# Kernel tuning notes

Measured on AMD Instinct MI355X. Metric: run time of the kernel, lower is better.

The kernel has to match this reference:

```python
import jax, jax.numpy as jnp
import numpy as np

N_NODES = 50000


def gcn_conv(x, edge_index, edge_weight, W, b):
    """PyG GCNConv: x' = D^{-1/2}(A+I)D^{-1/2} (x W) + b, with edge weights."""
    n = x.shape[0]
    x = x @ W  # transform first (PyG order): [N, d_out]
    row, col = edge_index[0], edge_index[1]  # source -> target
    # add self loops with weight 1
    loop = jnp.arange(n)
    row = jnp.concatenate([row, loop])
    col = jnp.concatenate([col, loop])
    ew = jnp.concatenate([edge_weight, jnp.ones((n,), dtype=x.dtype)])
    # symmetric normalization based on (weighted) in-degree at targets
    deg = jax.ops.segment_sum(ew, col, num_segments=n)
    dis = jnp.where(deg > 0, jax.lax.rsqrt(deg), 0.0)
    norm = dis[row] * ew * dis[col]  # [E+N]
    # gather-scale-scatter aggregation
    msg = x[row] * norm[:, None]  # [E+N, d_out]
    out = jax.ops.segment_sum(msg, col, num_segments=n)
    return out + b


def setup_inputs() -> dict:
    key = jax.random.key(0)
    ks = jax.random.split(key, 9)
    E = 800000
    bert_output = jax.random.normal(ks[0], (N_NODES, 1024), dtype=jnp.float32)
    edge_index = jax.random.randint(ks[1], (2, E), 0, N_NODES, dtype=jnp.int64)
    edge_weight = jax.random.uniform(ks[2], (E,), dtype=jnp.float32)
    s1 = 1.0 / np.sqrt(1024)
    s2 = 1.0 / np.sqrt(512)
    s3 = 1.0 / np.sqrt(128)
    W1 = jax.random.uniform(ks[3], (1024, 512), jnp.float32, -s1, s1)
    b1 = jnp.zeros((512,), jnp.float32)
    W2 = jax.random.uniform(ks[4], (512, 128), jnp.float32, -s2, s2)
    b2 = jnp.zeros((128,), jnp.float32)
    Wfc = jax.random.uniform(ks[5], (128, 14), jnp.float32, -s3, s3)
    bfc = jax.random.uniform(ks[6], (14,), jnp.float32, -s3, s3)
    return {
        "bert_output": bert_output,
        "edge_index": edge_index,
        "edge_weight": edge_weight,
        "W1": W1, "b1": b1, "W2": W2, "b2": b2, "Wfc": Wfc, "bfc": bfc,
    }


def reference(bert_output, edge_index, edge_weight, W1, b1, W2, b2, Wfc, bfc):
    h = jax.nn.relu(gcn_conv(bert_output, edge_index, edge_weight, W1, b1))
    h = jax.nn.relu(gcn_conv(h, edge_index, edge_weight, W2, b2))
    logits = h @ Wfc + bfc
    return jax.nn.sigmoid(logits)
```

## Files before the change

kernel.cpp:

```cpp
#include <hip/hip_runtime.h>
#include <stdint.h>

__device__ __forceinline__ float bf2f(unsigned short h) {
  union { uint32_t u; float f; } v; v.u = ((uint32_t)h) << 16; return v.f;
}
__device__ __forceinline__ unsigned short f2bf(float f) {
  union { float f; uint32_t u; } v; v.f = f;
  uint32_t u = v.u;
  u += 0x7FFFu + ((u >> 16) & 1u);
  return (unsigned short)(u >> 16);
}
__device__ __forceinline__ uint32_t pack2bf(float a, float b) {
  return (uint32_t)f2bf(a) | ((uint32_t)f2bf(b) << 16);
}

typedef __attribute__((ext_vector_type(8))) short short8;
typedef __attribute__((ext_vector_type(4))) float floatx4;

__device__ __forceinline__ void gl2lds16(const unsigned short* g, unsigned short* l) {
  __builtin_amdgcn_global_load_lds(
      (const __attribute__((address_space(1))) uint32_t*)(const void*)g,
      (__attribute__((address_space(3))) uint32_t*)(void*)l,
      16, 0, 0);
}

__global__ void bgcn_probe(const uint32_t* __restrict__ xw,
                           const uint32_t* __restrict__ iw,
                           int* __restrict__ flags) {
  if (threadIdx.x == 0 && blockIdx.x == 0) {
    int hits = 0;
    for (int i = 0; i < 256; ++i) {
      uint32_t b = (xw[i] >> 8) & 0x7F;
      if (b >= 0x38 && b <= 0x41) hits++;
    }
    flags[0] = (hits < 128) ? 1 : 0;
    int nz = 0;
    for (int i = 1; i < 128; i += 2) nz += (iw[i] != 0);
    flags[1] = (nz == 0) ? 1 : 0;
  }
}

__global__ void bgcn_cvt_f(const void* __restrict__ src, unsigned short* __restrict__ dst,
                           int n, const int* __restrict__ flags) {
  int i = blockIdx.x * 256 + threadIdx.x;
  if (i >= n) return;
  if (flags[0]) dst[i] = f2bf(((const float*)src)[i]);
  else          dst[i] = ((const unsigned short*)src)[i];
}
__global__ void bgcn_cvt8(const void* __restrict__ src, unsigned short* __restrict__ dst,
                          int n8, const int* __restrict__ flags) {
  int i = blockIdx.x * 256 + threadIdx.x;
  if (i >= n8) return;
  size_t o = (size_t)i * 8;
  uint4 d;
  if (flags[0]) {
    const float4* f = (const float4*)((const float*)src + o);
    float4 f0 = f[0], f1 = f[1];
    d = make_uint4(pack2bf(f0.x, f0.y), pack2bf(f0.z, f0.w),
                   pack2bf(f1.x, f1.y), pack2bf(f1.z, f1.w));
  } else {
    d = *(const uint4*)((const unsigned short*)src + o);
  }
  *(uint4*)(dst + o) = d;
}
__global__ void bgcn_cvt_i(const void* __restrict__ src, int* __restrict__ dst,
                           int n, const int* __restrict__ flags) {
  int i = blockIdx.x * 256 + threadIdx.x;
  if (i >= n) return;
  if (flags[1]) dst[i] = (int)((const long long*)src)[i];
  else          dst[i] = ((const int*)src)[i];
}
__global__ void bgcn_cvt_t(const void* __restrict__ src, unsigned short* __restrict__ dst,
                           int kbits, int N, int total, const int* __restrict__ flags) {
  int i = blockIdx.x * 256 + threadIdx.x;
  if (i >= total) return;
  int K = 1 << kbits;
  int n = i >> kbits;
  int k = i & (K - 1);
  size_t s = (size_t)k * N + n;
  if (flags[0]) dst[i] = f2bf(((const float*)src)[s]);
  else          dst[i] = ((const unsigned short*)src)[s];
}

__global__ void bgcn_init_deg(float* __restrict__ deg, int n) {
  int i = blockIdx.x * 256 + threadIdx.x;
  if (i < n) deg[i] = 1.0f;
}
__global__ void bgcn_deg(const int* __restrict__ col, const unsigned short* __restrict__ ew,
                         float* __restrict__ deg, int E) {
  int e = blockIdx.x * 256 + threadIdx.x;
  if (e < E) atomicAdd(&deg[col[e]], bf2f(ew[e]));
}
__global__ void bgcn_dis(const float* __restrict__ deg, float* __restrict__ dis, int n) {
  int i = blockIdx.x * 256 + threadIdx.x;
  if (i < n) dis[i] = rsqrtf(deg[i]);
}

__global__ void bgcn_hist(const int* __restrict__ col, int* __restrict__ counts, int E) {
  int e = blockIdx.x * 256 + threadIdx.x;
  if (e < E) atomicAdd(&counts[col[e]], 1);
}
__global__ void bgcn_scan_block(const int* __restrict__ counts, int* __restrict__ rowptr,
                                int* __restrict__ blocksum, int n) {
  __shared__ int buf[1024];
  int gid = blockIdx.x * 1024 + threadIdx.x;
  int v = (gid < n) ? counts[gid] : 0;
  buf[threadIdx.x] = v;
  __syncthreads();
  for (int off = 1; off < 1024; off <<= 1) {
    int x = (threadIdx.x >= off) ? buf[threadIdx.x - off] : 0;
    __syncthreads();
    buf[threadIdx.x] += x;
    __syncthreads();
  }
  if (gid < n) rowptr[gid + 1] = buf[threadIdx.x];
  if (threadIdx.x == 1023) blocksum[blockIdx.x] = buf[1023];
}
__global__ void bgcn_scan_tops(int* __restrict__ blocksum, int nb) {
  if (threadIdx.x == 0 && blockIdx.x == 0) {
    int acc = 0;
    for (int i = 0; i < nb; ++i) { int v = blocksum[i]; blocksum[i] = acc; acc += v; }
  }
}
__global__ void bgcn_scan_add(int* __restrict__ rowptr, const int* __restrict__ blocksum, int n) {
  int gid = blockIdx.x * 1024 + threadIdx.x;
  if (gid < n) rowptr[gid + 1] += blocksum[blockIdx.x];
  if (gid == 0) rowptr[0] = 0;
}
__global__ void bgcn_scatter(const int* __restrict__ row, const int* __restrict__ col,
                             const unsigned short* __restrict__ ew,
                             const float* __restrict__ dis,
                             const int* __restrict__ rowptr, int* __restrict__ fill,
                             int* __restrict__ esrc, float* __restrict__ enorm, int E) {
  int e = blockIdx.x * 256 + threadIdx.x;
  if (e >= E) return;
  int r = row[e], c = col[e];
  int pos = rowptr[c] + atomicAdd(&fill[c], 1);
  esrc[pos]  = r;
  enorm[pos] = dis[r] * bf2f(ew[e]) * dis[c];
}

__global__ __launch_bounds__(256) void bgcn_gemm_lds(
    const unsigned short* __restrict__ A,
    const unsigned short* __restrict__ Bt,
    unsigned short* __restrict__ C,
    int M, int N, int K, int nblk_bits) {
  __shared__ unsigned short Abuf[128 * 32];
  __shared__ unsigned short Bbuf[128 * 32];
  int t = threadIdx.x;
  int wave = t >> 6, lane = t & 63;
  int bx = blockIdx.x;
  int nblk = bx & ((1 << nblk_bits) - 1);
  int mblk = bx >> nblk_bits;
  int m0 = mblk * 128, n0 = nblk * 128;

  floatx4 acc[4][4];
  #pragma unroll
  for (int i = 0; i < 4; ++i)
    #pragma unroll
    for (int j = 0; j < 4; ++j)
      #pragma unroll
      for (int r = 0; r < 4; ++r) acc[i][j][r] = 0.0f;

  int rii  = lane >> 2;
  int koff = (lane & 3) * 8;
  int ar0 = m0 + wave * 32 + rii;      if (ar0 >= M) ar0 = M - 1;
  int ar1 = m0 + wave * 32 + 16 + rii; if (ar1 >= M) ar1 = M - 1;
  const unsigned short* Ag0 = A + (size_t)ar0 * K + koff;
  const unsigned short* Ag1 = A + (size_t)ar1 * K + koff;
  const unsigned short* Bg0 = Bt + (size_t)(n0 + wave * 32 + rii) * K + koff;
  const unsigned short* Bg1 = Bg0 + (size_t)16 * K;
  unsigned short* Al0 = Abuf + (wave * 32) * 32 + lane * 8;
  unsigned short* Al1 = Abuf + (wave * 32 + 16) * 32 + lane * 8;
  unsigned short* Bl0 = Bbuf + (wave * 32) * 32 + lane * 8;
  unsigned short* Bl1 = Bbuf + (wave * 32 + 16) * 32 + lane * 8;

  int fr = lane & 15;
  int fk = (lane >> 4) * 8;
  int mw = (wave & 1) * 64;
  int nw = (wave >> 1) * 64;

  for (int k0 = 0; k0 < K; k0 += 32) {
    gl2lds16(Ag0 + k0, Al0);
    gl2lds16(Ag1 + k0, Al1);
    gl2lds16(Bg0 + k0, Bl0);
    gl2lds16(Bg1 + k0, Bl1);
    __syncthreads();

    short8 afr[4], bfr[4];
    #pragma unroll
    for (int i = 0; i < 4; ++i)
      afr[i] = *(const short8*)(Abuf + (mw + i * 16 + fr) * 32 + fk);
    #pragma unroll
    for (int i = 0; i < 4; ++i)
      bfr[i] = *(const short8*)(Bbuf + (nw + i * 16 + fr) * 32 + fk);
    #pragma unroll
    for (int mt = 0; mt < 4; ++mt)
      #pragma unroll
      for (int nt = 0; nt < 4; ++nt)
        acc[mt][nt] = __builtin_amdgcn_mfma_f32_16x16x32_bf16(afr[mt], bfr[nt], acc[mt][nt], 0, 0, 0);
    __syncthreads();
  }

  int col_l = lane & 15;
  int row_b = (lane >> 4) * 4;
  #pragma unroll
  for (int mt = 0; mt < 4; ++mt)
    #pragma unroll
    for (int nt = 0; nt < 4; ++nt)
      #pragma unroll
      for (int r = 0; r < 4; ++r) {
        int m = m0 + mw + mt * 16 + row_b + r;
        if (m < M)
          C[(size_t)m * N + n0 + nw + nt * 16 + col_l] = f2bf(acc[mt][nt][r]);
      }
}

#define GST 40
__global__ __launch_bounds__(256, 2) void bgcn_gemm128(
    const void* __restrict__ Araw, int a_probe, const int* __restrict__ flags,
    const unsigned short* __restrict__ Bt,
    unsigned short* __restrict__ C,
    int M, int N, int K, int nblk_bits) {
  __shared__ unsigned short Abuf[128 * GST];
  __shared__ unsigned short Bbuf[128 * GST];
  const bool a_fp32 = a_probe && flags[0];
  int t = threadIdx.x;
  int wave = t >> 6, lane = t & 63;
  int bx = blockIdx.x;
  int nblk = bx & ((1 << nblk_bits) - 1);
  int mblk = bx >> nblk_bits;
  int m0 = mblk * 128, n0 = nblk * 128;

  floatx4 acc[4][4];
  #pragma unroll
  for (int i = 0; i < 4; ++i)
    #pragma unroll
    for (int j = 0; j < 4; ++j)
      #pragma unroll
      for (int r = 0; r < 4; ++r) acc[i][j][r] = 0.0f;

  int srow  = t >> 1;
  int skoff = (t & 1) * 16;
  int am = m0 + srow; if (am >= M) am = M - 1;
  const float*          Af = (const float*)Araw          + (size_t)am * K + skoff;
  const unsigned short* Ah = (const unsigned short*)Araw + (size_t)am * K + skoff;
  const unsigned short* Bp = Bt + (size_t)(n0 + srow) * K + skoff;
  unsigned short* AL = Abuf + srow * GST + skoff;
  unsigned short* BL = Bbuf + srow * GST + skoff;

  int fr = lane & 15;
  int fk = (lane >> 4) * 8;
  int mw = (wave & 1) * 64;
  int nw = (wave >> 1) * 64;

  for (int k0 = 0; k0 < K; k0 += 32) {
    uint4 a0, a1;
    if (a_fp32) {
      float4 f0 = *(const float4*)(Af + k0);
      float4 f1 = *(const float4*)(Af + k0 + 4);
      float4 f2 = *(const float4*)(Af + k0 + 8);
      float4 f3 = *(const float4*)(Af + k0 + 12);
      a0 = make_uint4(pack2bf(f0.x, f0.y), pack2bf(f0.z, f0.w),
                      pack2bf(f1.x, f1.y), pack2bf(f1.z, f1.w));
      a1 = make_uint4(pack2bf(f2.x, f2.y), pack2bf(f2.z, f2.w),
                      pack2bf(f3.x, f3.y), pack2bf(f3.z, f3.w));
    } else {
      a0 = *(const uint4*)(Ah + k0);
      a1 = *(const uint4*)(Ah + k0 + 8);
    }
    uint4 b0 = *(const uint4*)(Bp + k0);
    uint4 b1 = *(const uint4*)(Bp + k0 + 8);
    *(uint4*)AL       = a0;
    *(uint4*)(AL + 8) = a1;
    *(uint4*)BL       = b0;
    *(uint4*)(BL + 8) = b1;
    __syncthreads();

    short8 afr[4], bfr[4];
    #pragma unroll
    for (int i = 0; i < 4; ++i)
      afr[i] = *(const short8*)(Abuf + (mw + i * 16 + fr) * GST + fk);
    #pragma unroll
    for (int i = 0; i < 4; ++i)
      bfr[i] = *(const short8*)(Bbuf + (nw + i * 16 + fr) * GST + fk);
    #pragma unroll
    for (int mt = 0; mt < 4; ++mt)
      #pragma unroll
      for (int nt = 0; nt < 4; ++nt)
        acc[mt][nt] = __builtin_amdgcn_mfma_f32_16x16x32_bf16(afr[mt], bfr[nt], acc[mt][nt], 0, 0, 0);
    __syncthreads();
  }

  int col_l = lane & 15;
  int row_b = (lane >> 4) * 4;
  #pragma unroll
  for (int mt = 0; mt < 4; ++mt)
    #pragma unroll
    for (int nt = 0; nt < 4; ++nt)
      #pragma unroll
      for (int r = 0; r < 4; ++r) {
        int m = m0 + mw + mt * 16 + row_b + r;
        if (m < M)
          C[(size_t)m * N + n0 + nw + nt * 16 + col_l] = f2bf(acc[mt][nt][r]);
      }
}

template <int VPL>
__device__ __forceinline__ void loadbf(const unsigned short* p, float* out) {
  if constexpr (VPL == 8) {
    uint4 v = *(const uint4*)p;
    uint32_t w0 = v.x, w1 = v.y, w2 = v.z, w3 = v.w;
    out[0] = bf2f((unsigned short)(w0 & 0xffff)); out[1] = bf2f((unsigned short)(w0 >> 16));
    out[2] = bf2f((unsigned short)(w1 & 0xffff)); out[3] = bf2f((unsigned short)(w1 >> 16));
    out[4] = bf2f((unsigned short)(w2 & 0xffff)); out[5] = bf2f((unsigned short)(w2 >> 16));
    out[6] = bf2f((unsigned short)(w3 & 0xffff)); out[7] = bf2f((unsigned short)(w3 >> 16));
  } else {
    uint32_t v = *(const uint32_t*)p;
    out[0] = bf2f((unsigned short)(v & 0xffff)); out[1] = bf2f((unsigned short)(v >> 16));
  }
}

template <int F>
__global__ __launch_bounds__(256) void bgcn_aggregate(
    const unsigned short* __restrict__ H,
    const int* __restrict__ rowptr,
    const int* __restrict__ esrc,
    const float* __restrict__ enorm,
    const float* __restrict__ dis,
    const unsigned short* __restrict__ bias,
    unsigned short* __restrict__ Out,
    int n_nodes) {
  constexpr int VPL = F / 64;
  int lane = threadIdx.x & 63;
  int c = blockIdx.x * 4 + (threadIdx.x >> 6);
  if (c >= n_nodes) return;
  float acc[VPL];
  #pragma unroll
  for (int j = 0; j < VPL; ++j) acc[j] = 0.0f;

  int beg = rowptr[c], end = rowptr[c + 1];
  int e = beg;
  for (; e + 4 <= end; e += 4) {
    int s0 = esrc[e], s1 = esrc[e + 1], s2 = esrc[e + 2], s3 = esrc[e + 3];
    float w0 = enorm[e], w1 = enorm[e + 1], w2 = enorm[e + 2], w3 = enorm[e + 3];
    float v0[VPL], v1[VPL], v2[VPL], v3[VPL];
    loadbf<VPL>(H + (size_t)s0 * F + lane * VPL, v0);
    loadbf<VPL>(H + (size_t)s1 * F + lane * VPL, v1);
    loadbf<VPL>(H + (size_t)s2 * F + lane * VPL, v2);
    loadbf<VPL>(H + (size_t)s3 * F + lane * VPL, v3);
    #pragma unroll
    for (int j = 0; j < VPL; ++j) {
      acc[j] += w0 * v0[j];
      acc[j] += w1 * v1[j];
      acc[j] += w2 * v2[j];
      acc[j] += w3 * v3[j];
    }
  }
  for (; e < end; ++e) {
    int src = esrc[e];
    float w = enorm[e];
    float vals[VPL];
    loadbf<VPL>(H + (size_t)src * F + lane * VPL, vals);
    #pragma unroll
    for (int j = 0; j < VPL; ++j) acc[j] += w * vals[j];
  }
  float ds = dis[c];
  float wself = ds * ds;
  float vals[VPL];
  loadbf<VPL>(H + (size_t)c * F + lane * VPL, vals);
  unsigned short ob[VPL];
  #pragma unroll
  for (int j = 0; j < VPL; ++j) {
    float v = acc[j] + wself * vals[j] + bf2f(bias[lane * VPL + j]);
    ob[j] = f2bf(fmaxf(v, 0.0f));
  }
  if constexpr (VPL == 8) {
    uint4 st = make_uint4((uint32_t)ob[0] | ((uint32_t)ob[1] << 16),
                          (uint32_t)ob[2] | ((uint32_t)ob[3] << 16),
                          (uint32_t)ob[4] | ((uint32_t)ob[5] << 16),
                          (uint32_t)ob[6] | ((uint32_t)ob[7] << 16));
    *(uint4*)(Out + (size_t)c * F + lane * VPL) = st;
  } else {
    *(uint32_t*)(Out + (size_t)c * F + lane * VPL) =
        (uint32_t)ob[0] | ((uint32_t)ob[1] << 16);
  }
}

__global__ __launch_bounds__(256) void bgcn_fc_sigmoid(
    const unsigned short* __restrict__ X,
    const unsigned short* __restrict__ W,
    const unsigned short* __restrict__ b,
    float* __restrict__ out,
    int n_nodes) {
  __shared__ float Ws[128 * 14];
  __shared__ float bs[14];
  for (int i = threadIdx.x; i < 128 * 14; i += 256) Ws[i] = bf2f(W[i]);
  if (threadIdx.x < 14) bs[threadIdx.x] = bf2f(b[threadIdx.x]);
  __syncthreads();
  int node = blockIdx.x * 256 + threadIdx.x;
  if (node >= n_nodes) return;
  float acc[14];
  #pragma unroll
  for (int c = 0; c < 14; ++c) acc[c] = bs[c];
  const unsigned short* xp = X + (size_t)node * 128;
  for (int k8 = 0; k8 < 16; ++k8) {
    float xv[8];
    loadbf<8>(xp + k8 * 8, xv);
    #pragma unroll
    for (int j = 0; j < 8; ++j) {
      int k = k8 * 8 + j;
      #pragma unroll
      for (int c = 0; c < 14; ++c) acc[c] = fmaf(xv[j], Ws[k * 14 + c], acc[c]);
    }
  }
  float* op = out + (size_t)node * 14;
  #pragma unroll
  for (int c = 0; c < 14; ++c)
    op[c] = 1.0f / (1.0f + __expf(-acc[c]));
}

static inline size_t padsz(size_t x) { return (x + 255) & ~(size_t)255; }
static inline void* wsa(char*& p, size_t bytes) {
  void* r = p;
  p += padsz(bytes);
  return r;
}

extern "C" void kernel_launch(void* const* d_in, const int* in_sizes, int n_in,
                              void* d_out, int out_size, void* d_ws, size_t ws_size,
                              hipStream_t stream) {
  const void* Xr   = d_in[0];
  const void* EIr  = d_in[1];
  const void* EWr  = d_in[2];
  const void* W1r  = d_in[3];
  const void* b1r  = d_in[4];
  const void* W2r  = d_in[5];
  const void* b2r  = d_in[6];
  const void* Wfcr = d_in[7];
  const void* bfcr = d_in[8];
  float* out = (float*)d_out;

  const int N = in_sizes[0] / 1024;
  const int E = in_sizes[2];

  size_t need = padsz((size_t)N * 512 * 2)
              + padsz((size_t)N * 1024 * 2)
              + 4 * padsz((size_t)N * 4)
              + padsz((size_t)(N + 1) * 4)
              + padsz(256 * 4)
              + 2 * padsz((size_t)E * 4)
              + padsz((size_t)2 * E * 4)
              + padsz((size_t)E * 2)
              + padsz(1024 * 512 * 2) + padsz(512 * 128 * 2)
              + padsz(512 * 2) + padsz(128 * 2) + padsz(128 * 14 * 2)
              + padsz(32) + padsz(8);
  const bool big = ws_size >= need;

  char* p = (char*)d_ws;
  unsigned short* R1  = (unsigned short*)wsa(p, (size_t)N * 512 * 2);
  unsigned short* R2  = (unsigned short*)wsa(p, (size_t)N * (big ? 1024 : 512) * 2);
  float* deg      = (float*)wsa(p, (size_t)N * 4);
  float* dis      = (float*)wsa(p, (size_t)N * 4);
  int*   counts   = (int*)wsa(p, (size_t)N * 4);
  int*   fill     = (int*)wsa(p, (size_t)N * 4);
  int*   rowptr   = (int*)wsa(p, (size_t)(N + 1) * 4);
  int*   blocksum = (int*)wsa(p, 256 * 4);
  int*   esrc     = (int*)wsa(p, (size_t)E * 4);
  float* enorm    = (float*)wsa(p, (size_t)E * 4);
  int*   eidx     = (int*)wsa(p, (size_t)2 * E * 4);
  unsigned short* ewb  = (unsigned short*)wsa(p, (size_t)E * 2);
  unsigned short* W1t  = (unsigned short*)wsa(p, (size_t)1024 * 512 * 2);
  unsigned short* W2t  = (unsigned short*)wsa(p, (size_t)512 * 128 * 2);
  unsigned short* b1c  = (unsigned short*)wsa(p, 512 * 2);
  unsigned short* b2c  = (unsigned short*)wsa(p, 128 * 2);
  unsigned short* Wfcc = (unsigned short*)wsa(p, 128 * 14 * 2);
  unsigned short* bfcc = (unsigned short*)wsa(p, 32);
  int* flags      = (int*)wsa(p, 8);

  unsigned short* H1  = R1;
  unsigned short* Xbf = R2;
  unsigned short* X2  = R2;
  unsigned short* H2  = R1;
  unsigned short* X3  = R1 + (size_t)N * 128;

  int gN = (N + 255) / 256;
  int gE = (E + 255) / 256;

  bgcn_probe<<<1, 64, 0, stream>>>((const uint32_t*)Xr, (const uint32_t*)EIr, flags);
  bgcn_cvt_i<<<(2 * E + 255) / 256, 256, 0, stream>>>(EIr, eidx, 2 * E, flags);
  bgcn_cvt_f<<<gE, 256, 0, stream>>>(EWr, ewb, E, flags);
  bgcn_cvt_t<<<(1024 * 512 + 255) / 256, 256, 0, stream>>>(W1r, W1t, 10, 512, 1024 * 512, flags);
  bgcn_cvt_t<<<(512 * 128 + 255) / 256, 256, 0, stream>>>(W2r, W2t, 9, 128, 512 * 128, flags);
  bgcn_cvt_f<<<2, 256, 0, stream>>>(b1r, b1c, 512, flags);
  bgcn_cvt_f<<<1, 256, 0, stream>>>(b2r, b2c, 128, flags);
  bgcn_cvt_f<<<7, 256, 0, stream>>>(Wfcr, Wfcc, 128 * 14, flags);
  bgcn_cvt_f<<<1, 64, 0, stream>>>(bfcr, bfcc, 14, flags);
  if (big) {
    int n8 = N * 1024 / 8;
    bgcn_cvt8<<<(n8 + 255) / 256, 256, 0, stream>>>(Xr, Xbf, n8, flags);
  }

  const int* rowp = eidx;
  const int* colp = eidx + E;

  hipMemsetAsync(counts, 0, (size_t)N * 4, stream);
  hipMemsetAsync(fill,   0, (size_t)N * 4, stream);

  bgcn_init_deg<<<gN, 256, 0, stream>>>(deg, N);
  bgcn_deg<<<gE, 256, 0, stream>>>(colp, ewb, deg, E);
  bgcn_dis<<<gN, 256, 0, stream>>>(deg, dis, N);
  bgcn_hist<<<gE, 256, 0, stream>>>(colp, counts, E);

  int nb = (N + 1023) / 1024;
  bgcn_scan_block<<<nb, 1024, 0, stream>>>(counts, rowptr, blocksum, N);
  bgcn_scan_tops<<<1, 64, 0, stream>>>(blocksum, nb);
  bgcn_scan_add<<<nb, 1024, 0, stream>>>(rowptr, blocksum, N);
  bgcn_scatter<<<gE, 256, 0, stream>>>(rowp, colp, ewb, dis, rowptr, fill, esrc, enorm, E);

  int mblks = (N + 127) / 128;

  if (big)
    bgcn_gemm_lds<<<mblks * 4, 256, 0, stream>>>(Xbf, W1t, H1, N, 512, 1024, 2);
  else
    bgcn_gemm128<<<mblks * 4, 256, 0, stream>>>(Xr, 1, flags, W1t, H1, N, 512, 1024, 2);
  bgcn_aggregate<512><<<(N + 3) / 4, 256, 0, stream>>>(H1, rowptr, esrc, enorm, dis, b1c, X2, N);

  bgcn_gemm_lds<<<mblks, 256, 0, stream>>>(X2, W2t, H2, N, 128, 512, 0);
  bgcn_aggregate<128><<<(N + 3) / 4, 256, 0, stream>>>(H2, rowptr, esrc, enorm, dis, b2c, X3, N);

  bgcn_fc_sigmoid<<<gN, 256, 0, stream>>>(X3, Wfcc, bfcc, out, N);
}
```

Baseline: 780.9 us.

## Fuse preprocessing kernels, read raw edge inputs, tile weight transpose, widen gather unroll

```diff
diff --git a/kernel.cpp b/kernel.cpp
--- a/kernel.cpp
+++ b/kernel.cpp
@@ -12,6 +12,12 @@
 }
 __device__ __forceinline__ uint32_t pack2bf(float a, float b) {
   return (uint32_t)f2bf(a) | ((uint32_t)f2bf(b) << 16);
+}
+__device__ __forceinline__ int ld_idx(const void* p, size_t i, int is64) {
+  return is64 ? (int)((const long long*)p)[i] : ((const int*)p)[i];
+}
+__device__ __forceinline__ float ld_w(const void* p, size_t i, int f32) {
+  return f32 ? ((const float*)p)[i] : bf2f(((const unsigned short*)p)[i]);
 }
 
 typedef __attribute__((ext_vector_type(8))) short short8;
@@ -40,13 +46,6 @@
   }
 }
 
-__global__ void bgcn_cvt_f(const void* __restrict__ src, unsigned short* __restrict__ dst,
-                           int n, const int* __restrict__ flags) {
-  int i = blockIdx.x * 256 + threadIdx.x;
-  if (i >= n) return;
-  if (flags[0]) dst[i] = f2bf(((const float*)src)[i]);
-  else          dst[i] = ((const unsigned short*)src)[i];
-}
 __global__ void bgcn_cvt8(const void* __restrict__ src, unsigned short* __restrict__ dst,
                           int n8, const int* __restrict__ flags) {
   int i = blockIdx.x * 256 + threadIdx.x;
@@ -63,42 +62,57 @@
   }
   *(uint4*)(dst + o) = d;
 }
-__global__ void bgcn_cvt_i(const void* __restrict__ src, int* __restrict__ dst,
-                           int n, const int* __restrict__ flags) {
+__global__ __launch_bounds__(256) void bgcn_cvt_t(
+    const void* __restrict__ src, unsigned short* __restrict__ dst,
+    int K, int N, const int* __restrict__ flags) {
+  __shared__ unsigned short tile[32][33];
+  int k0 = blockIdx.x * 32, n0 = blockIdx.y * 32;
+  int tx = threadIdx.x & 31, ty = threadIdx.x >> 5;
+  bool f32 = flags[0];
+  #pragma unroll
+  for (int i = 0; i < 4; ++i) {
+    size_t s = (size_t)(k0 + ty + i * 8) * N + n0 + tx;
+    tile[ty + i * 8][tx] = f32 ? f2bf(((const float*)src)[s])
+                               : ((const unsigned short*)src)[s];
+  }
+  __syncthreads();
+  #pragma unroll
+  for (int i = 0; i < 4; ++i)
+    dst[(size_t)(n0 + ty + i * 8) * K + k0 + tx] = tile[tx][ty + i * 8];
+}
+__global__ void bgcn_cvt_small(const void* b1, const void* b2,
+                               const void* wfc, const void* bfc,
+                               unsigned short* db1, unsigned short* db2,
+                               unsigned short* dwfc, unsigned short* dbfc,
+                               const int* __restrict__ flags) {
   int i = blockIdx.x * 256 + threadIdx.x;
-  if (i >= n) return;
-  if (flags[1]) dst[i] = (int)((const long long*)src)[i];
-  else          dst[i] = ((const int*)src)[i];
-}
-__global__ void bgcn_cvt_t(const void* __restrict__ src, unsigned short* __restrict__ dst,
-                           int kbits, int N, int total, const int* __restrict__ flags) {
+  bool f32 = flags[0];
+  const void* s; unsigned short* d; int j;
+  if (i < 512)            { s = b1;  d = db1;  j = i; }
+  else if (i < 640)       { s = b2;  d = db2;  j = i - 512; }
+  else if (i < 2432)      { s = wfc; d = dwfc; j = i - 640; }
+  else if (i < 2446)      { s = bfc; d = dbfc; j = i - 2432; }
+  else return;
+  d[j] = f32 ? f2bf(((const float*)s)[j]) : ((const unsigned short*)s)[j];
+}
+
+__global__ void bgcn_init(float* __restrict__ deg, int* __restrict__ counts,
+                          int* __restrict__ fill, int n) {
   int i = blockIdx.x * 256 + threadIdx.x;
-  if (i >= total) return;
-  int K = 1 << kbits;
-  int n = i >> kbits;
-  int k = i & (K - 1);
-  size_t s = (size_t)k * N + n;
-  if (flags[0]) dst[i] = f2bf(((const float*)src)[s]);
-  else          dst[i] = ((const unsigned short*)src)[s];
-}
-
-__global__ void bgcn_init_deg(float* __restrict__ deg, int n) {
-  int i = blockIdx.x * 256 + threadIdx.x;
-  if (i < n) deg[i] = 1.0f;
-}
-__global__ void bgcn_deg(const int* __restrict__ col, const unsigned short* __restrict__ ew,
-                         float* __restrict__ deg, int E) {
+  if (i < n) { deg[i] = 1.0f; counts[i] = 0; fill[i] = 0; }
+}
+__global__ void bgcn_deg_hist(const void* __restrict__ ei, const void* __restrict__ ew,
+                              const int* __restrict__ flags,
+                              float* __restrict__ deg, int* __restrict__ counts, int E) {
   int e = blockIdx.x * 256 + threadIdx.x;
-  if (e < E) atomicAdd(&deg[col[e]], bf2f(ew[e]));
+  if (e >= E) return;
+  int c = ld_idx(ei, (size_t)E + e, flags[1]);
+  atomicAdd(&deg[c], ld_w(ew, e, flags[0]));
+  atomicAdd(&counts[c], 1);
 }
 __global__ void bgcn_dis(const float* __restrict__ deg, float* __restrict__ dis, int n) {
   int i = blockIdx.x * 256 + threadIdx.x;
   if (i < n) dis[i] = rsqrtf(deg[i]);
-}
-
-__global__ void bgcn_hist(const int* __restrict__ col, int* __restrict__ counts, int E) {
-  int e = blockIdx.x * 256 + threadIdx.x;
-  if (e < E) atomicAdd(&counts[col[e]], 1);
 }
 __global__ void bgcn_scan_block(const int* __restrict__ counts, int* __restrict__ rowptr,
                                 int* __restrict__ blocksum, int n) {
@@ -127,17 +141,18 @@
   if (gid < n) rowptr[gid + 1] += blocksum[blockIdx.x];
   if (gid == 0) rowptr[0] = 0;
 }
-__global__ void bgcn_scatter(const int* __restrict__ row, const int* __restrict__ col,
-                             const unsigned short* __restrict__ ew,
+__global__ void bgcn_scatter(const void* __restrict__ ei, const void* __restrict__ ew,
+                             const int* __restrict__ flags,
                              const float* __restrict__ dis,
                              const int* __restrict__ rowptr, int* __restrict__ fill,
                              int* __restrict__ esrc, float* __restrict__ enorm, int E) {
   int e = blockIdx.x * 256 + threadIdx.x;
   if (e >= E) return;
-  int r = row[e], c = col[e];
+  int is64 = flags[1];
+  int r = ld_idx(ei, e, is64), c = ld_idx(ei, (size_t)E + e, is64);
   int pos = rowptr[c] + atomicAdd(&fill[c], 1);
   esrc[pos]  = r;
-  enorm[pos] = dis[r] * bf2f(ew[e]) * dis[c];
+  enorm[pos] = dis[r] * ld_w(ew, e, flags[0]) * dis[c];
 }
 
 __global__ __launch_bounds__(256) void bgcn_gemm_lds(
@@ -306,19 +321,19 @@
       }
 }
 
-template <int VPL>
-__device__ __forceinline__ void loadbf(const unsigned short* p, float* out) {
-  if constexpr (VPL == 8) {
-    uint4 v = *(const uint4*)p;
-    uint32_t w0 = v.x, w1 = v.y, w2 = v.z, w3 = v.w;
-    out[0] = bf2f((unsigned short)(w0 & 0xffff)); out[1] = bf2f((unsigned short)(w0 >> 16));
-    out[2] = bf2f((unsigned short)(w1 & 0xffff)); out[3] = bf2f((unsigned short)(w1 >> 16));
-    out[4] = bf2f((unsigned short)(w2 & 0xffff)); out[5] = bf2f((unsigned short)(w2 >> 16));
-    out[6] = bf2f((unsigned short)(w3 & 0xffff)); out[7] = bf2f((unsigned short)(w3 >> 16));
-  } else {
-    uint32_t v = *(const uint32_t*)p;
-    out[0] = bf2f((unsigned short)(v & 0xffff)); out[1] = bf2f((unsigned short)(v >> 16));
-  }
+__device__ __forceinline__ void accum8(float* acc, uint4 r, float w) {
+  acc[0] += w * bf2f((unsigned short)(r.x & 0xffff));
+  acc[1] += w * bf2f((unsigned short)(r.x >> 16));
+  acc[2] += w * bf2f((unsigned short)(r.y & 0xffff));
+  acc[3] += w * bf2f((unsigned short)(r.y >> 16));
+  acc[4] += w * bf2f((unsigned short)(r.z & 0xffff));
+  acc[5] += w * bf2f((unsigned short)(r.z >> 16));
+  acc[6] += w * bf2f((unsigned short)(r.w & 0xffff));
+  acc[7] += w * bf2f((unsigned short)(r.w >> 16));
+}
+__device__ __forceinline__ void accum2(float* acc, uint32_t r, float w) {
+  acc[0] += w * bf2f((unsigned short)(r & 0xffff));
+  acc[1] += w * bf2f((unsigned short)(r >> 16));
 }
 
 template <int F>
@@ -340,39 +355,48 @@
   for (int j = 0; j < VPL; ++j) acc[j] = 0.0f;
 
   int beg = rowptr[c], end = rowptr[c + 1];
-  int e = beg;
-  for (; e + 4 <= end; e += 4) {
-    int s0 = esrc[e], s1 = esrc[e + 1], s2 = esrc[e + 2], s3 = esrc[e + 3];
-    float w0 = enorm[e], w1 = enorm[e + 1], w2 = enorm[e + 2], w3 = enorm[e + 3];
-    float v0[VPL], v1[VPL], v2[VPL], v3[VPL];
-    loadbf<VPL>(H + (size_t)s0 * F + lane * VPL, v0);
-    loadbf<VPL>(H + (size_t)s1 * F + lane * VPL, v1);
-    loadbf<VPL>(H + (size_t)s2 * F + lane * VPL, v2);
-    loadbf<VPL>(H + (size_t)s3 * F + lane * VPL, v3);
-    #pragma unroll
-    for (int j = 0; j < VPL; ++j) {
-      acc[j] += w0 * v0[j];
-      acc[j] += w1 * v1[j];
-      acc[j] += w2 * v2[j];
-      acc[j] += w3 * v3[j];
+  const unsigned short* Hl = H + (size_t)lane * VPL;
+
+  if (end > beg) {
+    for (int e = beg; e < end; e += 8) {
+      int   s[8]; float w[8];
+      #pragma unroll
+      for (int q = 0; q < 8; ++q) {
+        int idx = e + q;
+        int ii  = idx < end ? idx : end - 1;
+        s[q] = esrc[ii];
+        w[q] = idx < end ? enorm[ii] : 0.0f;
+      }
+      if constexpr (VPL == 8) {
+        uint4 r[8];
+        #pragma unroll
+        for (int q = 0; q < 8; ++q) r[q] = *(const uint4*)(Hl + (size_t)s[q] * F);
+        #pragma unroll
+        for (int q = 0; q < 8; ++q) accum8(acc, r[q], w[q]);
+      } else {
+        uint32_t r[8];
+        #pragma unroll
+        for (int q = 0; q < 8; ++q) r[q] = *(const uint32_t*)(Hl + (size_t)s[q] * F);
+        #pragma unroll
+        for (int q = 0; q < 8; ++q) accum2(acc, r[q], w[q]);
+      }
     }
   }
-  for (; e < end; ++e) {
-    int src = esrc[e];
-    float w = enorm[e];
-    float vals[VPL];
-    loadbf<VPL>(H + (size_t)src * F + lane * VPL, vals);
-    #pragma unroll
-    for (int j = 0; j < VPL; ++j) acc[j] += w * vals[j];
-  }
+
   float ds = dis[c];
   float wself = ds * ds;
-  float vals[VPL];
-  loadbf<VPL>(H + (size_t)c * F + lane * VPL, vals);
+  if constexpr (VPL == 8) {
+    uint4 rs = *(const uint4*)(Hl + (size_t)c * F);
+    accum8(acc, rs, wself);
+  } else {
+    uint32_t rs = *(const uint32_t*)(Hl + (size_t)c * F);
+    accum2(acc, rs, wself);
+  }
+
   unsigned short ob[VPL];
   #pragma unroll
   for (int j = 0; j < VPL; ++j) {
-    float v = acc[j] + wself * vals[j] + bf2f(bias[lane * VPL + j]);
+    float v = acc[j] + bf2f(bias[lane * VPL + j]);
     ob[j] = f2bf(fmaxf(v, 0.0f));
   }
   if constexpr (VPL == 8) {
@@ -405,8 +429,12 @@
   for (int c = 0; c < 14; ++c) acc[c] = bs[c];
   const unsigned short* xp = X + (size_t)node * 128;
   for (int k8 = 0; k8 < 16; ++k8) {
+    uint4 r = *(const uint4*)(xp + k8 * 8);
     float xv[8];
-    loadbf<8>(xp + k8 * 8, xv);
+    xv[0] = bf2f((unsigned short)(r.x & 0xffff)); xv[1] = bf2f((unsigned short)(r.x >> 16));
+    xv[2] = bf2f((unsigned short)(r.y & 0xffff)); xv[3] = bf2f((unsigned short)(r.y >> 16));
+    xv[4] = bf2f((unsigned short)(r.z & 0xffff)); xv[5] = bf2f((unsigned short)(r.z >> 16));
+    xv[6] = bf2f((unsigned short)(r.w & 0xffff)); xv[7] = bf2f((unsigned short)(r.w >> 16));
     #pragma unroll
     for (int j = 0; j < 8; ++j) {
       int k = k8 * 8 + j;
@@ -450,8 +478,6 @@
               + padsz((size_t)(N + 1) * 4)
               + padsz(256 * 4)
               + 2 * padsz((size_t)E * 4)
-              + padsz((size_t)2 * E * 4)
-              + padsz((size_t)E * 2)
               + padsz(1024 * 512 * 2) + padsz(512 * 128 * 2)
               + padsz(512 * 2) + padsz(128 * 2) + padsz(128 * 14 * 2)
               + padsz(32) + padsz(8);
@@ -468,8 +494,6 @@
   int*   blocksum = (int*)wsa(p, 256 * 4);
   int*   esrc     = (int*)wsa(p, (size_t)E * 4);
   float* enorm    = (float*)wsa(p, (size_t)E * 4);
-  int*   eidx     = (int*)wsa(p, (size_t)2 * E * 4);
-  unsigned short* ewb  = (unsigned short*)wsa(p, (size_t)E * 2);
   unsigned short* W1t  = (unsigned short*)wsa(p, (size_t)1024 * 512 * 2);
   unsigned short* W2t  = (unsigned short*)wsa(p, (size_t)512 * 128 * 2);
   unsigned short* b1c  = (unsigned short*)wsa(p, 512 * 2);
@@ -488,35 +512,22 @@
   int gE = (E + 255) / 256;
 
   bgcn_probe<<<1, 64, 0, stream>>>((const uint32_t*)Xr, (const uint32_t*)EIr, flags);
-  bgcn_cvt_i<<<(2 * E + 255) / 256, 256, 0, stream>>>(EIr, eidx, 2 * E, flags);
-  bgcn_cvt_f<<<gE, 256, 0, stream>>>(EWr, ewb, E, flags);
-  bgcn_cvt_t<<<(1024 * 512 + 255) / 256, 256, 0, stream>>>(W1r, W1t, 10, 512, 1024 * 512, flags);
-  bgcn_cvt_t<<<(512 * 128 + 255) / 256, 256, 0, stream>>>(W2r, W2t, 9, 128, 512 * 128, flags);
-  bgcn_cvt_f<<<2, 256, 0, stream>>>(b1r, b1c, 512, flags);
-  bgcn_cvt_f<<<1, 256, 0, stream>>>(b2r, b2c, 128, flags);
-  bgcn_cvt_f<<<7, 256, 0, stream>>>(Wfcr, Wfcc, 128 * 14, flags);
-  bgcn_cvt_f<<<1, 64, 0, stream>>>(bfcr, bfcc, 14, flags);
+  { dim3 g(1024 / 32, 512 / 32); bgcn_cvt_t<<<g, 256, 0, stream>>>(W1r, W1t, 1024, 512, flags); }
+  { dim3 g(512 / 32, 128 / 32);  bgcn_cvt_t<<<g, 256, 0, stream>>>(W2r, W2t, 512, 128, flags); }
+  bgcn_cvt_small<<<10, 256, 0, stream>>>(b1r, b2r, Wfcr, bfcr, b1c, b2c, Wfcc, bfcc, flags);
   if (big) {
     int n8 = N * 1024 / 8;
     bgcn_cvt8<<<(n8 + 255) / 256, 256, 0, stream>>>(Xr, Xbf, n8, flags);
   }
 
-  const int* rowp = eidx;
-  const int* colp = eidx + E;
-
-  hipMemsetAsync(counts, 0, (size_t)N * 4, stream);
-  hipMemsetAsync(fill,   0, (size_t)N * 4, stream);
-
-  bgcn_init_deg<<<gN, 256, 0, stream>>>(deg, N);
-  bgcn_deg<<<gE, 256, 0, stream>>>(colp, ewb, deg, E);
+  bgcn_init<<<gN, 256, 0, stream>>>(deg, counts, fill, N);
+  bgcn_deg_hist<<<gE, 256, 0, stream>>>(EIr, EWr, flags, deg, counts, E);
   bgcn_dis<<<gN, 256, 0, stream>>>(deg, dis, N);
-  bgcn_hist<<<gE, 256, 0, stream>>>(colp, counts, E);
-
   int nb = (N + 1023) / 1024;
   bgcn_scan_block<<<nb, 1024, 0, stream>>>(counts, rowptr, blocksum, N);
   bgcn_scan_tops<<<1, 64, 0, stream>>>(blocksum, nb);
   bgcn_scan_add<<<nb, 1024, 0, stream>>>(rowptr, blocksum, N);
-  bgcn_scatter<<<gE, 256, 0, stream>>>(rowp, colp, ewb, dis, rowptr, fill, esrc, enorm, E);
+  bgcn_scatter<<<gE, 256, 0, stream>>>(EIr, EWr, flags, dis, rowptr, fill, esrc, enorm, E);
 
   int mblks = (N + 127) / 128;
 
```

Result: faster. 742.6 us (-4.9%).
